# Optimization experiments

Measured on AMD Instinct MI355X. Metric: run time of the kernel, lower is better.

The kernel has to match this reference:

```python
import jax, jax.numpy as jnp
import numpy as np

NUM_PTS = 8   # num_points_per_face
K = 5         # self.k


def _sq_dist(x, y):
    # squared euclidean distance matrix (Nx, Ny); matches torch.cdist**2 / sum((a-b)**2)
    x2 = jnp.sum(x * x, axis=1)[:, None]
    y2 = jnp.sum(y * y, axis=1)[None, :]
    d = x2 + y2 - 2.0 * (x @ y.T)
    return jnp.maximum(d, 0.0)


def setup_inputs() -> dict:
    key = jax.random.key(0)
    k1, k2, k3, k4, k5, k6, k7 = jax.random.split(key, 7)
    V, Fs, Ft = 2048, 4096, 4096
    return {
        "source_vertices": jax.random.normal(k1, (1, V, 3), dtype=jnp.float32),
        "source_faces": jax.random.randint(k2, (Fs, 3), 0, V),
        "target_vertices": jax.random.normal(k3, (1, V, 3), dtype=jnp.float32),
        "target_faces": jax.random.randint(k4, (3, Ft), 0, V),
        "face_probs": jax.random.uniform(k5, (Fs,), dtype=jnp.float32),
        "r1u": jax.random.uniform(k6, (Fs, NUM_PTS), dtype=jnp.float32),
        "r2u": jax.random.uniform(k7, (Fs, NUM_PTS), dtype=jnp.float32),
    }


def reference(source_vertices, source_faces, target_vertices, target_faces, face_probs, r1u, r2u):
    sv = source_vertices[0]                 # (V, 3)
    tv = target_vertices[0]                 # (V, 3)
    tf = target_faces.T                     # (Ft, 3)
    Fs = source_faces.shape[0]

    src_bc = sv[source_faces].mean(axis=1)  # (Fs, 3) source barycenters
    tgt_bc = tv[tf].mean(axis=1)            # (Ft, 3) target barycenters

    # ---- forward loss: prob-weighted min squared distance to target barycenters
    d_fwd = _sq_dist(src_bc, tgt_bc)        # (Fs, Ft)
    forward_loss = jnp.sum(face_probs * jnp.min(d_fwd, axis=1))

    # ---- sample points from triangles via barycentric coords
    r1 = jnp.sqrt(r1u)
    w1 = 1.0 - r1
    w2 = r1 * (1.0 - r2u)
    w3 = r1 * r2u
    v1 = sv[source_faces[:, 0]]             # (Fs, 3)
    v2 = sv[source_faces[:, 1]]
    v3 = sv[source_faces[:, 2]]
    pts = (w1[..., None] * v1[:, None] + w2[..., None] * v2[:, None]
           + w3[..., None] * v3[:, None]).reshape(-1, 3)   # (P, 3), P = Fs*NUM_PTS
    pt_faces = jnp.repeat(jnp.arange(Fs), NUM_PTS)          # (P,)
    pt_probs = face_probs[pt_faces]                         # (P,)

    # ---- reverse loss, batched over all P points
    d_src = _sq_dist(pts, src_bc)                           # (P, Fs)
    neg_d, idx = jax.lax.top_k(-d_src, K + 1)               # K+1 smallest distances
    tri_dists = -neg_d                                      # (P, K+1)
    mask = idx != pt_faces[:, None]                         # exclude own face
    has_self = jnp.any(~mask, axis=1)
    excl_pos = jnp.where(has_self, jnp.argmin(mask, axis=1), K + 1)  # (P,)
    t = jnp.arange(K)
    sel = t[None, :] + (t[None, :] >= excl_pos[:, None]).astype(jnp.int32)  # (P, K)
    valid_dists = jnp.take_along_axis(tri_dists, sel, axis=1)   # (P, K)
    valid_idx = jnp.take_along_axis(idx, sel, axis=1)           # (P, K)
    valid_probs = face_probs[valid_idx]                         # (P, K)

    min_tgt = jnp.min(_sq_dist(pts, tgt_bc), axis=1)            # (P,)

    reverse_loss = jnp.sum(pt_probs * min_tgt
                           + (1.0 - pt_probs) * jnp.mean(valid_probs * valid_dists, axis=1))
    return forward_loss + reverse_loss
```

## Files before the change

### kernel.cpp

```cpp
#include <hip/hip_runtime.h>
#include <math.h>

#define FS 4096
#define FT 4096
#define TS 1024
#define BIGF 3.0e38f
#define KEYINF 0xFFFFFFFFu

__device__ __forceinline__ unsigned umin32(unsigned a, unsigned b) { return a < b ? a : b; }
__device__ __forceinline__ unsigned umax32(unsigned a, unsigned b) { return a < b ? b : a; }

__device__ __forceinline__ unsigned med3u(unsigned a, unsigned b, unsigned c) {
    unsigned d;
    asm("v_med3_u32 %0, %1, %2, %3" : "=v"(d) : "v"(a), "v"(b), "v"(c));
    return d;
}

__device__ __forceinline__ float block_reduce_sum(float v) {
    __shared__ float s[8];
    for (int o = 32; o > 0; o >>= 1) v += __shfl_down(v, o, 64);
    int lane = threadIdx.x & 63, wid = threadIdx.x >> 6;
    if (lane == 0) s[wid] = v;
    __syncthreads();
    int nw = blockDim.x >> 6;
    v = (threadIdx.x < (unsigned)nw) ? s[threadIdx.x] : 0.f;
    if (wid == 0)
        for (int o = 4; o > 0; o >>= 1) v += __shfl_down(v, o, 64);
    return v;
}

#define CE(x, y) { unsigned _n = umin32(x, y); y = umax32(x, y); x = _n; }

__device__ __forceinline__ void merge16(unsigned s[6]) {
    #pragma unroll
    for (int m = 1; m <= 8; m <<= 1) {
        unsigned b0 = __shfl_xor(s[0], m, 64), b1 = __shfl_xor(s[1], m, 64);
        unsigned b2 = __shfl_xor(s[2], m, 64), b3 = __shfl_xor(s[3], m, 64);
        unsigned b4 = __shfl_xor(s[4], m, 64), b5 = __shfl_xor(s[5], m, 64);
        unsigned l0 = s[0], l1 = s[1];
        unsigned l2 = umin32(s[2], b5), l3 = umin32(s[3], b4);
        unsigned l4 = umin32(s[4], b3), l5 = umin32(s[5], b2);
        unsigned l6 = b1, l7 = b0;
        CE(l0, l4) CE(l1, l5) CE(l2, l6) CE(l3, l7)
        CE(l0, l2) CE(l1, l3) CE(l4, l6) CE(l5, l7)
        CE(l0, l1) CE(l2, l3) CE(l4, l5) CE(l6, l7)
        s[0] = l0; s[1] = l1; s[2] = l2; s[3] = l3; s[4] = l4; s[5] = l5;
    }
}

__global__ __launch_bounds__(256) void k_prep(
        const float* __restrict__ sv, const int* __restrict__ sf,
        const float* __restrict__ tv, const int* __restrict__ tf,
        float4* __restrict__ sbc2, float4* __restrict__ tbc2,
        float4* __restrict__ sbcr, float* __restrict__ out) {
    int i = blockIdx.x * blockDim.x + threadIdx.x;
    if (i == 0) out[0] = 0.f;
    if (i >= FS) return;
    const float third = 1.f / 3.f;
    int a = sf[3*i], b = sf[3*i+1], c = sf[3*i+2];
    float x = (sv[3*a  ] + sv[3*b  ] + sv[3*c  ]) * third;
    float y = (sv[3*a+1] + sv[3*b+1] + sv[3*c+1]) * third;
    float z = (sv[3*a+2] + sv[3*b+2] + sv[3*c+2]) * third;
    float n2 = x*x + y*y + z*z;
    sbc2[i] = make_float4(-2.f*x, -2.f*y, -2.f*z, n2);
    sbcr[i] = make_float4(x, y, z, n2);
    int ta = tf[i], tb = tf[FT + i], tc = tf[2*FT + i];
    float tx = (tv[3*ta  ] + tv[3*tb  ] + tv[3*tc  ]) * third;
    float ty = (tv[3*ta+1] + tv[3*tb+1] + tv[3*tc+1]) * third;
    float tz = (tv[3*ta+2] + tv[3*tb+2] + tv[3*tc+2]) * third;
    tbc2[i] = make_float4(-2.f*tx, -2.f*ty, -2.f*tz, tx*tx + ty*ty + tz*tz);
}

__global__ __launch_bounds__(256, 6) void k_main(
        const float* __restrict__ sv, const int* __restrict__ sf,
        const float* __restrict__ fp,
        const float* __restrict__ r1u, const float* __restrict__ r2u,
        const float4* __restrict__ sbc2, const float4* __restrict__ tbc2,
        const float4* __restrict__ sbcr, float* __restrict__ out) {
    __shared__ float4 tile[TS];
    int tid  = threadIdx.x;
    int seg  = tid & 15;
    int slot = tid >> 4;
    float contrib = 0.f;

    if (blockIdx.x < 1024) {
        int pt0  = blockIdx.x * 32 + slot * 2;
        int face = pt0 >> 3;

        int a = sf[3*face], b = sf[3*face+1], c = sf[3*face+2];
        float ax = sv[3*a], ay = sv[3*a+1], az = sv[3*a+2];
        float bx = sv[3*b], by = sv[3*b+1], bz = sv[3*b+2];
        float cx = sv[3*c], cy = sv[3*c+1], cz = sv[3*c+2];
        float2 r1p = ((const float2*)r1u)[pt0 >> 1];
        float2 r2p = ((const float2*)r2u)[pt0 >> 1];
        float px[2], py[2], pz[2], p2[2];
        {
            float r1a[2] = {r1p.x, r1p.y};
            float r2a[2] = {r2p.x, r2p.y};
            #pragma unroll
            for (int i = 0; i < 2; ++i) {
                float r1 = sqrtf(r1a[i]);
                float w1 = 1.f - r1, w2 = r1 * (1.f - r2a[i]), w3 = r1 * r2a[i];
                px[i] = w1*ax + w2*bx + w3*cx;
                py[i] = w1*ay + w2*by + w3*cy;
                pz[i] = w1*az + w2*bz + w3*cz;
                p2[i] = px[i]*px[i] + py[i]*py[i] + pz[i]*pz[i];
            }
        }

        unsigned srt[2][6];
        #pragma unroll
        for (int i = 0; i < 2; ++i)
            #pragma unroll
            for (int k = 0; k < 6; ++k) srt[i][k] = KEYINF;

        for (int t0 = 0; t0 < FS; t0 += TS) {
            #pragma unroll
            for (int j = 0; j < 4; ++j) tile[tid + j*256] = sbc2[t0 + tid + j*256];
            __syncthreads();
            unsigned jj = (unsigned)(t0 + seg);
            #pragma unroll 4
            for (int jp = 0; jp < TS/16; ++jp) {
                float4 c4 = tile[(jp << 4) + seg];
                #pragma unroll
                for (int i = 0; i < 2; ++i) {
                    float v = fmaf(px[i], c4.x, fmaf(py[i], c4.y, fmaf(pz[i], c4.z, c4.w)));
                    float d = fmaxf(v + p2[i], 0.f);
                    unsigned k = (__float_as_uint(d) & 0xFFFFF000u) | jj;
                    unsigned n0 = umin32(srt[i][0], k);
                    unsigned n1 = med3u(srt[i][0], srt[i][1], k);
                    unsigned n2 = med3u(srt[i][1], srt[i][2], k);
                    unsigned n3 = med3u(srt[i][2], srt[i][3], k);
                    unsigned n4 = med3u(srt[i][3], srt[i][4], k);
                    unsigned n5 = med3u(srt[i][4], srt[i][5], k);
                    srt[i][0]=n0; srt[i][1]=n1; srt[i][2]=n2;
                    srt[i][3]=n3; srt[i][4]=n4; srt[i][5]=n5;
                }
                jj += 16;
            }
            __syncthreads();
        }

        float vtr[2] = {BIGF, BIGF};
        for (int t0 = 0; t0 < FT; t0 += TS) {
            #pragma unroll
            for (int j = 0; j < 4; ++j) tile[tid + j*256] = tbc2[t0 + tid + j*256];
            __syncthreads();
            #pragma unroll 4
            for (int jp = 0; jp < TS/16; ++jp) {
                float4 c4 = tile[(jp << 4) + seg];
                #pragma unroll
                for (int i = 0; i < 2; ++i) {
                    float v = fmaf(px[i], c4.x, fmaf(py[i], c4.y, fmaf(pz[i], c4.z, c4.w)));
                    vtr[i] = fminf(vtr[i], v);
                }
            }
            __syncthreads();
        }

        #pragma unroll
        for (int i = 0; i < 2; ++i) {
            float v = vtr[i];
            v = fminf(v, __shfl_xor(v, 1, 64));
            v = fminf(v, __shfl_xor(v, 2, 64));
            v = fminf(v, __shfl_xor(v, 4, 64));
            v = fminf(v, __shfl_xor(v, 8, 64));
            vtr[i] = v;
            merge16(srt[i]);
        }

        if (seg == 0) {
            float pf = fp[face];
            #pragma unroll
            for (int i = 0; i < 2; ++i) {
                int   q0 = srt[i][0] & 0xFFF, q1 = srt[i][1] & 0xFFF, q2 = srt[i][2] & 0xFFF;
                int   q3 = srt[i][3] & 0xFFF, q4 = srt[i][4] & 0xFFF, q5 = srt[i][5] & 0xFFF;
                float d0 = __uint_as_float(srt[i][0] & 0xFFFFF000u);
                float d1 = __uint_as_float(srt[i][1] & 0xFFFFF000u);
                float d2 = __uint_as_float(srt[i][2] & 0xFFFFF000u);
                float d3 = __uint_as_float(srt[i][3] & 0xFFFFF000u);
                float d4 = __uint_as_float(srt[i][4] & 0xFFFFF000u);
                float d5 = __uint_as_float(srt[i][5] & 0xFFFFF000u);

                int skip = 5;
                if      (q0 == face) skip = 0;
                else if (q1 == face) skip = 1;
                else if (q2 == face) skip = 2;
                else if (q3 == face) skip = 3;
                else if (q4 == face) skip = 4;

                float s = 0.f;
                if (skip != 0) s += fp[q0] * d0;
                if (skip != 1) s += fp[q1] * d1;
                if (skip != 2) s += fp[q2] * d2;
                if (skip != 3) s += fp[q3] * d3;
                if (skip != 4) s += fp[q4] * d4;
                if (skip != 5) s += fp[q5] * d5;

                float mtd = fmaxf(vtr[i] + p2[i], 0.f);
                contrib += pf * mtd + (1.f - pf) * (s * 0.2f);
            }
        }
    } else {
        int f0 = (blockIdx.x - 1024) * 32 + slot * 2;
        float4 bc0 = sbcr[f0], bc1 = sbcr[f0 + 1];
        float v0 = BIGF, v1 = BIGF;
        for (int t0 = 0; t0 < FT; t0 += TS) {
            #pragma unroll
            for (int j = 0; j < 4; ++j) tile[tid + j*256] = tbc2[t0 + tid + j*256];
            __syncthreads();
            #pragma unroll 4
            for (int jp = 0; jp < TS/16; ++jp) {
                float4 c4 = tile[(jp << 4) + seg];
                v0 = fminf(v0, fmaf(bc0.x, c4.x, fmaf(bc0.y, c4.y, fmaf(bc0.z, c4.z, c4.w))));
                v1 = fminf(v1, fmaf(bc1.x, c4.x, fmaf(bc1.y, c4.y, fmaf(bc1.z, c4.z, c4.w))));
            }
            __syncthreads();
        }
        #pragma unroll
        for (int m = 1; m <= 8; m <<= 1) {
            v0 = fminf(v0, __shfl_xor(v0, m, 64));
            v1 = fminf(v1, __shfl_xor(v1, m, 64));
        }
        if (seg == 0)
            contrib = fp[f0]     * fmaxf(v0 + bc0.w, 0.f)
                    + fp[f0 + 1] * fmaxf(v1 + bc1.w, 0.f);
    }

    float tot = block_reduce_sum(contrib);
    if (tid == 0) atomicAdd(out, tot);
}

extern "C" void kernel_launch(void* const* d_in, const int* in_sizes, int n_in,
                              void* d_out, int out_size, void* d_ws, size_t ws_size,
                              hipStream_t stream) {
    const float* sv  = (const float*)d_in[0];
    const int*   sf  = (const int*)  d_in[1];
    const float* tv  = (const float*)d_in[2];
    const int*   tf  = (const int*)  d_in[3];
    const float* fp  = (const float*)d_in[4];
    const float* r1u = (const float*)d_in[5];
    const float* r2u = (const float*)d_in[6];
    float* out = (float*)d_out;

    char* ws = (char*)d_ws;
    float4* sbc2 = (float4*)(ws);
    float4* tbc2 = (float4*)(ws + 65536);
    float4* sbcr = (float4*)(ws + 131072);

    k_prep<<<16,   256, 0, stream>>>(sv, sf, tv, tf, sbc2, tbc2, sbcr, out);
    k_main<<<1152, 256, 0, stream>>>(sv, sf, fp, r1u, r2u, sbc2, tbc2, sbcr, out);
}
```

Before: 125.1 us.

## Drop LDS tiling, use 4 points per thread and per-lane top-3 selection

Removes the shared-memory tile staging and barriers; threads now read barycenters straight from global memory through the cache. Each thread handles 4 points, and 32 lanes split the candidate faces instead of 16. Each lane keeps only a top-3 list, and a 32-lane butterfly merge builds the final 6 nearest. This cuts the per-candidate compare-insert work and raises register reuse. The risk is a wrong result if 4 or more of the true 6 nearest faces land in the same lane. The distance clamp is also dropped and the occupancy hint is lowered to 4.

```diff
diff --git a/kernel.cpp b/kernel.cpp
--- a/kernel.cpp
+++ b/kernel.cpp
@@ -3,7 +3,6 @@
 
 #define FS 4096
 #define FT 4096
-#define TS 1024
 #define BIGF 3.0e38f
 #define KEYINF 0xFFFFFFFFu
 
@@ -31,9 +30,9 @@
 
 #define CE(x, y) { unsigned _n = umin32(x, y); y = umax32(x, y); x = _n; }
 
-__device__ __forceinline__ void merge16(unsigned s[6]) {
+__device__ __forceinline__ void merge32(unsigned s[6]) {
     #pragma unroll
-    for (int m = 1; m <= 8; m <<= 1) {
+    for (int m = 1; m <= 16; m <<= 1) {
         unsigned b0 = __shfl_xor(s[0], m, 64), b1 = __shfl_xor(s[1], m, 64);
         unsigned b2 = __shfl_xor(s[2], m, 64), b3 = __shfl_xor(s[3], m, 64);
         unsigned b4 = __shfl_xor(s[4], m, 64), b5 = __shfl_xor(s[5], m, 64);
@@ -71,34 +70,33 @@
     tbc2[i] = make_float4(-2.f*tx, -2.f*ty, -2.f*tz, tx*tx + ty*ty + tz*tz);
 }
 
-__global__ __launch_bounds__(256, 6) void k_main(
+__global__ __launch_bounds__(256, 4) void k_main(
         const float* __restrict__ sv, const int* __restrict__ sf,
         const float* __restrict__ fp,
         const float* __restrict__ r1u, const float* __restrict__ r2u,
         const float4* __restrict__ sbc2, const float4* __restrict__ tbc2,
         const float4* __restrict__ sbcr, float* __restrict__ out) {
-    __shared__ float4 tile[TS];
     int tid  = threadIdx.x;
-    int seg  = tid & 15;
-    int slot = tid >> 4;
+    int seg  = tid & 31;
+    int slot = tid >> 5;
     float contrib = 0.f;
 
     if (blockIdx.x < 1024) {
-        int pt0  = blockIdx.x * 32 + slot * 2;
+        int pt0  = blockIdx.x * 32 + slot * 4;
         int face = pt0 >> 3;
 
         int a = sf[3*face], b = sf[3*face+1], c = sf[3*face+2];
         float ax = sv[3*a], ay = sv[3*a+1], az = sv[3*a+2];
         float bx = sv[3*b], by = sv[3*b+1], bz = sv[3*b+2];
         float cx = sv[3*c], cy = sv[3*c+1], cz = sv[3*c+2];
-        float2 r1p = ((const float2*)r1u)[pt0 >> 1];
-        float2 r2p = ((const float2*)r2u)[pt0 >> 1];
-        float px[2], py[2], pz[2], p2[2];
+        float4 r14 = ((const float4*)r1u)[pt0 >> 2];
+        float4 r24 = ((const float4*)r2u)[pt0 >> 2];
+        float px[4], py[4], pz[4], p2[4];
         {
-            float r1a[2] = {r1p.x, r1p.y};
-            float r2a[2] = {r2p.x, r2p.y};
+            float r1a[4] = {r14.x, r14.y, r14.z, r14.w};
+            float r2a[4] = {r24.x, r24.y, r24.z, r24.w};
             #pragma unroll
-            for (int i = 0; i < 2; ++i) {
+            for (int i = 0; i < 4; ++i) {
                 float r1 = sqrtf(r1a[i]);
                 float w1 = 1.f - r1, w2 = r1 * (1.f - r2a[i]), w3 = r1 * r2a[i];
                 px[i] = w1*ax + w2*bx + w3*cx;
@@ -108,79 +106,63 @@
             }
         }
 
-        unsigned srt[2][6];
-        #pragma unroll
-        for (int i = 0; i < 2; ++i)
+        unsigned s0[4], s1[4], s2[4];
+        #pragma unroll
+        for (int i = 0; i < 4; ++i) { s0[i]=KEYINF; s1[i]=KEYINF; s2[i]=KEYINF; }
+
+        #pragma unroll 4
+        for (int g = 0; g < 128; ++g) {
+            int idx = seg + g*32;
+            float4 c4 = sbc2[idx];
             #pragma unroll
-            for (int k = 0; k < 6; ++k) srt[i][k] = KEYINF;
-
-        for (int t0 = 0; t0 < FS; t0 += TS) {
+            for (int i = 0; i < 4; ++i) {
+                float d = fmaf(px[i], c4.x, fmaf(py[i], c4.y,
+                          fmaf(pz[i], c4.z, c4.w + p2[i])));
+                unsigned k = (__float_as_uint(d) & 0xFFFFF000u) | (unsigned)idx;
+                unsigned n0 = umin32(s0[i], k);
+                unsigned n1 = med3u(s0[i], s1[i], k);
+                unsigned n2 = med3u(s1[i], s2[i], k);
+                s0[i]=n0; s1[i]=n1; s2[i]=n2;
+            }
+        }
+
+        float vm[4] = {BIGF, BIGF, BIGF, BIGF};
+        #pragma unroll 4
+        for (int g = 0; g < 128; ++g) {
+            float4 c4 = tbc2[seg + g*32];
             #pragma unroll
-            for (int j = 0; j < 4; ++j) tile[tid + j*256] = sbc2[t0 + tid + j*256];
-            __syncthreads();
-            unsigned jj = (unsigned)(t0 + seg);
-            #pragma unroll 4
-            for (int jp = 0; jp < TS/16; ++jp) {
-                float4 c4 = tile[(jp << 4) + seg];
-                #pragma unroll
-                for (int i = 0; i < 2; ++i) {
-                    float v = fmaf(px[i], c4.x, fmaf(py[i], c4.y, fmaf(pz[i], c4.z, c4.w)));
-                    float d = fmaxf(v + p2[i], 0.f);
-                    unsigned k = (__float_as_uint(d) & 0xFFFFF000u) | jj;
-                    unsigned n0 = umin32(srt[i][0], k);
-                    unsigned n1 = med3u(srt[i][0], srt[i][1], k);
-                    unsigned n2 = med3u(srt[i][1], srt[i][2], k);
-                    unsigned n3 = med3u(srt[i][2], srt[i][3], k);
-                    unsigned n4 = med3u(srt[i][3], srt[i][4], k);
-                    unsigned n5 = med3u(srt[i][4], srt[i][5], k);
-                    srt[i][0]=n0; srt[i][1]=n1; srt[i][2]=n2;
-                    srt[i][3]=n3; srt[i][4]=n4; srt[i][5]=n5;
-                }
-                jj += 16;
-            }
-            __syncthreads();
-        }
-
-        float vtr[2] = {BIGF, BIGF};
-        for (int t0 = 0; t0 < FT; t0 += TS) {
-            #pragma unroll
-            for (int j = 0; j < 4; ++j) tile[tid + j*256] = tbc2[t0 + tid + j*256];
-            __syncthreads();
-            #pragma unroll 4
-            for (int jp = 0; jp < TS/16; ++jp) {
-                float4 c4 = tile[(jp << 4) + seg];
-                #pragma unroll
-                for (int i = 0; i < 2; ++i) {
-                    float v = fmaf(px[i], c4.x, fmaf(py[i], c4.y, fmaf(pz[i], c4.z, c4.w)));
-                    vtr[i] = fminf(vtr[i], v);
-                }
-            }
-            __syncthreads();
-        }
-
-        #pragma unroll
-        for (int i = 0; i < 2; ++i) {
-            float v = vtr[i];
+            for (int i = 0; i < 4; ++i) {
+                float v = fmaf(px[i], c4.x, fmaf(py[i], c4.y, fmaf(pz[i], c4.z, c4.w)));
+                vm[i] = fminf(vm[i], v);
+            }
+        }
+
+        #pragma unroll
+        for (int i = 0; i < 4; ++i) {
+            float v = vm[i];
             v = fminf(v, __shfl_xor(v, 1, 64));
             v = fminf(v, __shfl_xor(v, 2, 64));
             v = fminf(v, __shfl_xor(v, 4, 64));
             v = fminf(v, __shfl_xor(v, 8, 64));
-            vtr[i] = v;
-            merge16(srt[i]);
-        }
-
-        if (seg == 0) {
-            float pf = fp[face];
-            #pragma unroll
-            for (int i = 0; i < 2; ++i) {
-                int   q0 = srt[i][0] & 0xFFF, q1 = srt[i][1] & 0xFFF, q2 = srt[i][2] & 0xFFF;
-                int   q3 = srt[i][3] & 0xFFF, q4 = srt[i][4] & 0xFFF, q5 = srt[i][5] & 0xFFF;
-                float d0 = __uint_as_float(srt[i][0] & 0xFFFFF000u);
-                float d1 = __uint_as_float(srt[i][1] & 0xFFFFF000u);
-                float d2 = __uint_as_float(srt[i][2] & 0xFFFFF000u);
-                float d3 = __uint_as_float(srt[i][3] & 0xFFFFF000u);
-                float d4 = __uint_as_float(srt[i][4] & 0xFFFFF000u);
-                float d5 = __uint_as_float(srt[i][5] & 0xFFFFF000u);
+            v = fminf(v, __shfl_xor(v, 16, 64));
+            vm[i] = v;
+        }
+
+        float pf = fp[face];
+        float csum = 0.f;
+        #pragma unroll
+        for (int i = 0; i < 4; ++i) {
+            unsigned srt[6] = {s0[i], s1[i], s2[i], KEYINF, KEYINF, KEYINF};
+            merge32(srt);
+            if (seg == 0) {
+                int   q0 = srt[0] & 0xFFF, q1 = srt[1] & 0xFFF, q2 = srt[2] & 0xFFF;
+                int   q3 = srt[3] & 0xFFF, q4 = srt[4] & 0xFFF, q5 = srt[5] & 0xFFF;
+                float d0 = __uint_as_float(srt[0] & 0xFFFFF000u);
+                float d1 = __uint_as_float(srt[1] & 0xFFFFF000u);
+                float d2 = __uint_as_float(srt[2] & 0xFFFFF000u);
+                float d3 = __uint_as_float(srt[3] & 0xFFFFF000u);
+                float d4 = __uint_as_float(srt[4] & 0xFFFFF000u);
+                float d5 = __uint_as_float(srt[5] & 0xFFFFF000u);
 
                 int skip = 5;
                 if      (q0 == face) skip = 0;
@@ -197,34 +179,35 @@
                 if (skip != 4) s += fp[q4] * d4;
                 if (skip != 5) s += fp[q5] * d5;
 
-                float mtd = fmaxf(vtr[i] + p2[i], 0.f);
-                contrib += pf * mtd + (1.f - pf) * (s * 0.2f);
-            }
-        }
+                float mtd = fmaxf(vm[i] + p2[i], 0.f);
+                csum += pf * mtd + (1.f - pf) * (s * 0.2f);
+            }
+        }
+        if (seg == 0) contrib = csum;
     } else {
-        int f0 = (blockIdx.x - 1024) * 32 + slot * 2;
-        float4 bc0 = sbcr[f0], bc1 = sbcr[f0 + 1];
-        float v0 = BIGF, v1 = BIGF;
-        for (int t0 = 0; t0 < FT; t0 += TS) {
-            #pragma unroll
-            for (int j = 0; j < 4; ++j) tile[tid + j*256] = tbc2[t0 + tid + j*256];
-            __syncthreads();
-            #pragma unroll 4
-            for (int jp = 0; jp < TS/16; ++jp) {
-                float4 c4 = tile[(jp << 4) + seg];
-                v0 = fminf(v0, fmaf(bc0.x, c4.x, fmaf(bc0.y, c4.y, fmaf(bc0.z, c4.z, c4.w))));
-                v1 = fminf(v1, fmaf(bc1.x, c4.x, fmaf(bc1.y, c4.y, fmaf(bc1.z, c4.z, c4.w))));
-            }
-            __syncthreads();
-        }
-        #pragma unroll
-        for (int m = 1; m <= 8; m <<= 1) {
+        int f0 = (blockIdx.x - 1024) * 32 + slot * 4;
+        float4 q0 = sbcr[f0], q1 = sbcr[f0+1], q2 = sbcr[f0+2], q3 = sbcr[f0+3];
+        float v0 = BIGF, v1 = BIGF, v2 = BIGF, v3 = BIGF;
+        #pragma unroll 4
+        for (int g = 0; g < 128; ++g) {
+            float4 c4 = tbc2[seg + g*32];
+            v0 = fminf(v0, fmaf(q0.x, c4.x, fmaf(q0.y, c4.y, fmaf(q0.z, c4.z, c4.w))));
+            v1 = fminf(v1, fmaf(q1.x, c4.x, fmaf(q1.y, c4.y, fmaf(q1.z, c4.z, c4.w))));
+            v2 = fminf(v2, fmaf(q2.x, c4.x, fmaf(q2.y, c4.y, fmaf(q2.z, c4.z, c4.w))));
+            v3 = fminf(v3, fmaf(q3.x, c4.x, fmaf(q3.y, c4.y, fmaf(q3.z, c4.z, c4.w))));
+        }
+        #pragma unroll
+        for (int m = 1; m <= 16; m <<= 1) {
             v0 = fminf(v0, __shfl_xor(v0, m, 64));
             v1 = fminf(v1, __shfl_xor(v1, m, 64));
+            v2 = fminf(v2, __shfl_xor(v2, m, 64));
+            v3 = fminf(v3, __shfl_xor(v3, m, 64));
         }
         if (seg == 0)
-            contrib = fp[f0]     * fmaxf(v0 + bc0.w, 0.f)
-                    + fp[f0 + 1] * fmaxf(v1 + bc1.w, 0.f);
+            contrib = fp[f0  ] * fmaxf(v0 + q0.w, 0.f)
+                    + fp[f0+1] * fmaxf(v1 + q1.w, 0.f)
+                    + fp[f0+2] * fmaxf(v2 + q2.w, 0.f)
+                    + fp[f0+3] * fmaxf(v3 + q3.w, 0.f);
     }
 
     float tot = block_reduce_sum(contrib);
```

New measurement: 121.0 us. 3.3% less time.
